# Optimization experiments

Hardware: AMD Instinct MI355X
Metric: run time of the kernel (lower is better)

## Reference

```python
import jax, jax.numpy as jnp
import numpy as np
from jax import lax

L, B, T, C, F = 4, 4, 2048, 1024, 4096  # n_layer, batch, ctx_len, n_embd(=dim_att), dim_ffn
EPS = 1e-5


def setup_inputs() -> dict:
    key = jax.random.key(0)
    ks = jax.random.split(key, 16)
    s = 0.02
    d = {}
    d["x"] = jax.random.normal(ks[0], (B, T, C), jnp.float32)
    d["ln0_w"] = jnp.ones((C,), jnp.float32)
    d["ln0_b"] = jnp.zeros((C,), jnp.float32)
    d["ln1_w"] = jnp.ones((L, C), jnp.float32)
    d["ln1_b"] = jnp.zeros((L, C), jnp.float32)
    d["ln2_w"] = jnp.ones((L, C), jnp.float32)
    d["ln2_b"] = jnp.zeros((L, C), jnp.float32)
    d["time_decay"] = jax.random.normal(ks[1], (L, C), jnp.float32) * 0.5
    d["time_first"] = jax.random.normal(ks[2], (L, C), jnp.float32) * 0.5 + jnp.float32(np.log(0.3))
    d["tmk"] = jax.random.uniform(ks[3], (L, C), jnp.float32)
    d["tmv"] = jax.random.uniform(ks[4], (L, C), jnp.float32)
    d["tmr"] = jax.random.uniform(ks[5], (L, C), jnp.float32)
    d["Wk"] = jax.random.normal(ks[6], (L, C, C), jnp.float32) * s
    d["Wv"] = jax.random.normal(ks[7], (L, C, C), jnp.float32) * s
    d["Wr"] = jax.random.normal(ks[8], (L, C, C), jnp.float32) * s
    d["Wo"] = jax.random.normal(ks[9], (L, C, C), jnp.float32) * s
    d["cmk"] = jax.random.uniform(ks[10], (L, C), jnp.float32)
    d["cmr"] = jax.random.uniform(ks[11], (L, C), jnp.float32)
    d["Wck"] = jax.random.normal(ks[12], (L, F, C), jnp.float32) * s  # key: n_embd -> dim_ffn
    d["Wcv"] = jax.random.normal(ks[13], (L, C, F), jnp.float32) * s  # value: dim_ffn -> n_embd
    d["Wcr"] = jax.random.normal(ks[14], (L, C, C), jnp.float32) * s  # receptance
    return d


def layernorm(x, w, b):
    m = jnp.mean(x, axis=-1, keepdims=True)
    v = jnp.var(x, axis=-1, keepdims=True)
    return (x - m) * lax.rsqrt(v + EPS) * w + b


def time_shift(x):
    # ZeroPad2d((0,0,1,-1)): shift sequence right by one, zero at t=0
    return jnp.pad(x, ((0, 0), (1, 0), (0, 0)))[:, :-1]


def wkv(time_decay, time_first, k, v):
    # numerically-stable RWKV-4 WKV recurrence; k,v: [B,T,C]
    w = -jnp.exp(time_decay)  # [C]
    u = time_first            # [C]
    kt = jnp.swapaxes(k, 0, 1)  # [T,B,C]
    vt = jnp.swapaxes(v, 0, 1)
    Bn, Cn = k.shape[0], k.shape[2]
    init = (jnp.zeros((Bn, Cn), k.dtype), jnp.zeros((Bn, Cn), k.dtype),
            jnp.full((Bn, Cn), -1e38, k.dtype))

    def step(carry, kv):
        aa, bb, pp = carry
        kk, vv = kv
        ww = u + kk
        qq = jnp.maximum(pp, ww)
        e1 = jnp.exp(pp - qq)
        e2 = jnp.exp(ww - qq)
        out = (e1 * aa + e2 * vv) / (e1 * bb + e2)
        ww2 = pp + w
        qq2 = jnp.maximum(ww2, kk)
        e1b = jnp.exp(ww2 - qq2)
        e2b = jnp.exp(kk - qq2)
        return (e1b * aa + e2b * vv, e1b * bb + e2b, qq2), out

    _, out = lax.scan(step, init, (kt, vt))
    return jnp.swapaxes(out, 0, 1)  # [B,T,C]


def reference(x, ln0_w, ln0_b, ln1_w, ln1_b, ln2_w, ln2_b, time_decay, time_first,
              tmk, tmv, tmr, Wk, Wv, Wr, Wo, cmk, cmr, Wck, Wcv, Wcr):
    x = layernorm(x, ln0_w, ln0_b)  # ln0 on layer 0
    for l in range(L):
        # --- TimeMix ---
        h = layernorm(x, ln1_w[l], ln1_b[l])
        hh = time_shift(h)
        xk = h * tmk[l] + hh * (1 - tmk[l])
        xv = h * tmv[l] + hh * (1 - tmv[l])
        xr = h * tmr[l] + hh * (1 - tmr[l])
        k = jnp.einsum('btc,oc->bto', xk, Wk[l])
        v = jnp.einsum('btc,oc->bto', xv, Wv[l])
        sr = jax.nn.sigmoid(jnp.einsum('btc,oc->bto', xr, Wr[l]))
        rwkv = sr * wkv(time_decay[l], time_first[l], k, v)
        x = x + jnp.einsum('bto,co->btc', rwkv, Wo[l])
        # --- ChannelMix ---
        h = layernorm(x, ln2_w[l], ln2_b[l])
        hh = time_shift(h)
        xk = h * cmk[l] + hh * (1 - cmk[l])
        xr = h * cmr[l] + hh * (1 - cmr[l])
        kf = jnp.einsum('btc,fc->btf', xk, Wck[l])
        kf = jnp.square(jax.nn.relu(kf))
        kv = jnp.einsum('btf,cf->btc', kf, Wcv[l])
        x = x + jax.nn.sigmoid(jnp.einsum('btc,oc->bto', xr, Wcr[l])) * kv
    return x
```

## Files before the change

### kernel.cpp

```cpp
#include <hip/hip_runtime.h>
#include <cstdint>

#define TT 2048
#define CCH 1024
#define FFD 4096
#define EPSV 1e-5f
#define NCHK 32
#define CHKL 64

typedef __attribute__((ext_vector_type(4))) float floatx4;
typedef __attribute__((ext_vector_type(8))) short shortx8;

__device__ __forceinline__ unsigned short f32_to_bf16(float f){
  union { float f; unsigned int u; } x; x.f = f;
  unsigned int r = x.u + 0x7fffu + ((x.u >> 16) & 1u);
  return (unsigned short)(r >> 16);
}
__device__ __forceinline__ float bf16_to_f32(unsigned short h){
  union { unsigned int u; float f; } x; x.u = ((unsigned int)h) << 16;
  return x.f;
}
__device__ __forceinline__ float wave_sum(float v){
  #pragma unroll
  for (int o = 32; o > 0; o >>= 1) v += __shfl_down(v, o, 64);
  return v;
}
__device__ __forceinline__ void async16(const void* g, void* l){
  __builtin_amdgcn_global_load_lds((const __attribute__((address_space(1))) void*)g,
                                   (__attribute__((address_space(3))) void*)l, 16, 0, 0);
}

__global__ __launch_bounds__(256) void cvt_kernel(const float* __restrict__ s,
                                                  unsigned short* __restrict__ d, int n4){
  int i = blockIdx.x * 256 + threadIdx.x;
  if (i >= n4) return;
  float4 v = ((const float4*)s)[i];
  union { unsigned short u[4]; uint2 p; } o;
  o.u[0] = f32_to_bf16(v.x); o.u[1] = f32_to_bf16(v.y);
  o.u[2] = f32_to_bf16(v.z); o.u[3] = f32_to_bf16(v.w);
  *(uint2*)&d[(long)i * 4] = o.p;
}

__global__ __launch_bounds__(256) void ln0_kernel(const float* __restrict__ xin,
    const float* __restrict__ w, const float* __restrict__ b, float* __restrict__ xo){
  const int row = blockIdx.x, tid = threadIdx.x;
  const float* xr = xin + (long)row * CCH;
  float c4[4]; float s = 0.f, s2 = 0.f;
  #pragma unroll
  for (int j = 0; j < 4; j++){ c4[j] = xr[tid + j*256]; s += c4[j]; s2 += c4[j]*c4[j]; }
  s = wave_sum(s); s2 = wave_sum(s2);
  __shared__ float red[2][4];
  const int wid = tid >> 6, lane = tid & 63;
  if (lane == 0){ red[0][wid] = s; red[1][wid] = s2; }
  __syncthreads();
  const float S  = red[0][0]+red[0][1]+red[0][2]+red[0][3];
  const float S2 = red[1][0]+red[1][1]+red[1][2]+red[1][3];
  const float inv = 1.f / CCH;
  const float m = S * inv;
  const float rs = rsqrtf(S2 * inv - m*m + EPSV);
  float* xout = xo + (long)row * CCH;
  #pragma unroll
  for (int j = 0; j < 4; j++){ int c = tid + j*256; xout[c] = (c4[j]-m)*rs*w[c] + b[c]; }
}

template<int NOUT>
__global__ __launch_bounds__(256) void ln_mix(
    const float* __restrict__ x,
    const float* __restrict__ lw, const float* __restrict__ lb,
    const float* __restrict__ mk, const float* __restrict__ mv, const float* __restrict__ mr,
    unsigned short* __restrict__ xk, unsigned short* __restrict__ xv, unsigned short* __restrict__ xr)
{
  const int row = blockIdx.x;
  const int t = row & (TT - 1);
  const int tid = threadIdx.x;
  const float* xc = x + (long)row * CCH;
  const float* xp = xc - CCH;
  float c4[4], p4[4];
  float s1=0.f, s2=0.f, s3=0.f, s4=0.f;
  #pragma unroll
  for (int j = 0; j < 4; j++){
    const int c = tid + j*256;
    c4[j] = xc[c];
    p4[j] = (t > 0) ? xp[c] : 0.f;
    s1 += c4[j]; s2 += c4[j]*c4[j];
    s3 += p4[j]; s4 += p4[j]*p4[j];
  }
  s1 = wave_sum(s1); s2 = wave_sum(s2); s3 = wave_sum(s3); s4 = wave_sum(s4);
  __shared__ float red[4][4];
  const int wid = tid >> 6, lane = tid & 63;
  if (lane == 0){ red[wid][0]=s1; red[wid][1]=s2; red[wid][2]=s3; red[wid][3]=s4; }
  __syncthreads();
  const float S1 = red[0][0]+red[1][0]+red[2][0]+red[3][0];
  const float S2 = red[0][1]+red[1][1]+red[2][1]+red[3][1];
  const float S3 = red[0][2]+red[1][2]+red[2][2]+red[3][2];
  const float S4 = red[0][3]+red[1][3]+red[2][3]+red[3][3];
  const float inv = 1.f / CCH;
  const float m1 = S1*inv; const float r1 = rsqrtf(S2*inv - m1*m1 + EPSV);
  const float m0 = S3*inv; const float r0 = rsqrtf(S4*inv - m0*m0 + EPSV);
  #pragma unroll
  for (int j = 0; j < 4; j++){
    const int c = tid + j*256;
    const long o = (long)row * CCH + c;
    const float wv = lw[c], bv = lb[c];
    const float h  = (c4[j]-m1)*r1*wv + bv;
    const float hp = (t > 0) ? ((p4[j]-m0)*r0*wv + bv) : 0.f;
    const float a = mk[c]; xk[o] = f32_to_bf16(h*a + hp*(1.f-a));
    if (NOUT == 3){ const float q = mv[c]; xv[o] = f32_to_bf16(h*q + hp*(1.f-q)); }
    const float g = mr[c]; xr[o] = f32_to_bf16(h*g + hp*(1.f-g));
  }
}

__global__ __launch_bounds__(256) void wkv_pass1(
    const unsigned short* __restrict__ kin, const unsigned short* __restrict__ vin,
    const float* __restrict__ td,
    float* __restrict__ sta, float* __restrict__ stb, float* __restrict__ stp)
{
  const int c = blockIdx.x * 256 + threadIdx.x;
  const int chunk = blockIdx.y, b = blockIdx.z;
  const float w = -__expf(td[c]);
  const long base = ((long)b * TT + (long)chunk * CHKL) * CCH + c;
  float aa = 0.f, bb = 0.f, pp = -1e38f;
  for (int t0 = 0; t0 < CHKL; t0 += 8) {
    float kr[8], vr[8];
    #pragma unroll
    for (int j = 0; j < 8; j++){
      const long o = base + (long)(t0 + j) * CCH;
      kr[j] = bf16_to_f32(kin[o]);
      vr[j] = bf16_to_f32(vin[o]);
    }
    #pragma unroll
    for (int j = 0; j < 8; j++){
      const float kk = kr[j], vv = vr[j];
      const float ww2 = pp + w;
      const float qq2 = fmaxf(ww2, kk);
      const float e1b = __expf(ww2 - qq2), e2b = __expf(kk - qq2);
      aa = e1b*aa + e2b*vv; bb = e1b*bb + e2b; pp = qq2;
    }
  }
  const long si = (long)chunk * 4096 + b * CCH + c;
  sta[si] = aa; stb[si] = bb; stp[si] = pp;
}

__global__ __launch_bounds__(256) void wkv_combine(
    const float* __restrict__ td,
    const float* __restrict__ sta, const float* __restrict__ stb, const float* __restrict__ stp,
    float* __restrict__ ina, float* __restrict__ inb, float* __restrict__ inp)
{
  const int idx = blockIdx.x * 256 + threadIdx.x;
  const int c = idx & (CCH - 1);
  const float wn = -__expf(td[c]) * (float)CHKL;
  float a = 0.f, b = 0.f, p = -1e38f;
  for (int j0 = 0; j0 < NCHK; j0 += 8) {
    float la[8], lb[8], lp[8];
    #pragma unroll
    for (int j = 0; j < 8; j++){
      const long si = (long)(j0 + j) * 4096 + idx;
      la[j] = sta[si]; lb[j] = stb[si]; lp[j] = stp[si];
    }
    #pragma unroll
    for (int j = 0; j < 8; j++){
      const long si = (long)(j0 + j) * 4096 + idx;
      ina[si] = a; inb[si] = b; inp[si] = p;
      const float pd = p + wn;
      const float q = fmaxf(pd, lp[j]);
      const float e1 = __expf(pd - q), e2 = __expf(lp[j] - q);
      a = e1*a + e2*la[j]; b = e1*b + e2*lb[j]; p = q;
    }
  }
}

__global__ __launch_bounds__(256) void wkv_pass2(
    const unsigned short* __restrict__ kin, const unsigned short* __restrict__ vin,
    const unsigned short* __restrict__ srin,
    const float* __restrict__ td, const float* __restrict__ tf,
    const float* __restrict__ ina, const float* __restrict__ inb, const float* __restrict__ inp,
    unsigned short* __restrict__ out)
{
  const int c = blockIdx.x * 256 + threadIdx.x;
  const int chunk = blockIdx.y, b = blockIdx.z;
  const float w = -__expf(td[c]);
  const float u = tf[c];
  const long si = (long)chunk * 4096 + b * CCH + c;
  float aa = ina[si], bb = inb[si], pp = inp[si];
  const long base = ((long)b * TT + (long)chunk * CHKL) * CCH + c;
  for (int t0 = 0; t0 < CHKL; t0 += 8) {
    float kr[8], vr[8], sr[8];
    #pragma unroll
    for (int j = 0; j < 8; j++){
      const long o = base + (long)(t0 + j) * CCH;
      kr[j] = bf16_to_f32(kin[o]);
      vr[j] = bf16_to_f32(vin[o]);
      sr[j] = bf16_to_f32(srin[o]);
    }
    #pragma unroll
    for (int j = 0; j < 8; j++){
      const float kk = kr[j], vv = vr[j];
      const float ww = u + kk;
      const float qq = fmaxf(pp, ww);
      const float e1 = __expf(pp - qq), e2 = __expf(ww - qq);
      const float outv = (e1*aa + e2*vv) / (e1*bb + e2);
      const float ww2 = pp + w;
      const float qq2 = fmaxf(ww2, kk);
      const float e1b = __expf(ww2 - qq2), e2b = __expf(kk - qq2);
      aa = e1b*aa + e2b*vv; bb = e1b*bb + e2b; pp = qq2;
      out[base + (long)(t0 + j) * CCH] = f32_to_bf16(sr[j] * outv);
    }
  }
}

#define BM 128
#define BN 128
#define BK 32

enum { EP_BF16 = 0, EP_SIG = 1, EP_RELU2 = 2, EP_ADD = 3, EP_MULADD = 4 };

template<int EPI>
__global__ __launch_bounds__(256) void gemm_bt(
    const unsigned short* __restrict__ A,
    const unsigned short* __restrict__ W,
    const int N, const int K,
    unsigned short* __restrict__ outb,
    float* __restrict__ xres,
    const unsigned short* __restrict__ rr)
{
  __shared__ unsigned short lA[BM * BK];
  __shared__ unsigned short lW[BN * BK];
  const int tid = threadIdx.x;
  const int bm = blockIdx.x, bn = blockIdx.y;
  const int wid = tid >> 6, lane = tid & 63;
  const int wm = (wid >> 1) * 64, wn = (wid & 1) * 64;
  const int quad = lane >> 4, r16 = lane & 15;

  const unsigned short* Ag = A + ((long)(bm * BM + (tid >> 2))) * K + (tid & 3) * 8;
  const unsigned short* Wg = W + ((long)(bn * BN + (tid >> 2))) * K + (tid & 3) * 8;
  const long rs64 = (long)64 * K;
  unsigned short* lA0 = &lA[wid * 512];
  unsigned short* lA1 = &lA[2048 + wid * 512];
  unsigned short* lW0 = &lW[wid * 512];
  unsigned short* lW1 = &lW[2048 + wid * 512];

  const floatx4 zf = {0.f, 0.f, 0.f, 0.f};
  floatx4 acc[4][4];
  #pragma unroll
  for (int i = 0; i < 4; i++)
    #pragma unroll
    for (int j = 0; j < 4; j++) acc[i][j] = zf;

  for (int k0 = 0; k0 < K; k0 += BK) {
    __syncthreads();
    async16(Ag + k0, lA0);
    async16(Ag + rs64 + k0, lA1);
    async16(Wg + k0, lW0);
    async16(Wg + rs64 + k0, lW1);
    __syncthreads();
    shortx8 af[4], bf[4];
    #pragma unroll
    for (int m = 0; m < 4; m++) af[m] = *(const shortx8*)&lA[(wm + m*16 + r16) * BK + quad * 8];
    #pragma unroll
    for (int n = 0; n < 4; n++) bf[n] = *(const shortx8*)&lW[(wn + n*16 + r16) * BK + quad * 8];
    #pragma unroll
    for (int m = 0; m < 4; m++)
      #pragma unroll
      for (int n = 0; n < 4; n++)
        acc[m][n] = __builtin_amdgcn_mfma_f32_16x16x32_bf16(af[m], bf[n], acc[m][n], 0, 0, 0);
  }

  const int colBase = bn * BN + wn + r16;
  #pragma unroll
  for (int m = 0; m < 4; m++) {
    const int rowBase = bm * BM + wm + m * 16 + quad * 4;
    #pragma unroll
    for (int n = 0; n < 4; n++) {
      const int col = colBase + n * 16;
      #pragma unroll
      for (int r = 0; r < 4; r++) {
        const long idx = (long)(rowBase + r) * N + col;
        const float val = acc[m][n][r];
        if (EPI == EP_BF16)      outb[idx] = f32_to_bf16(val);
        else if (EPI == EP_SIG)  outb[idx] = f32_to_bf16(1.f / (1.f + __expf(-val)));
        else if (EPI == EP_RELU2){ const float t = val > 0.f ? val : 0.f; outb[idx] = f32_to_bf16(t * t); }
        else if (EPI == EP_ADD)  xres[idx] += val;
        else                     xres[idx] = fmaf(bf16_to_f32(rr[idx]), val, xres[idx]);
      }
    }
  }
}

extern "C" void kernel_launch(void* const* d_in, const int* in_sizes, int n_in,
                              void* d_out, int out_size, void* d_ws, size_t ws_size,
                              hipStream_t stream)
{
  const float* x_in       = (const float*)d_in[0];
  const float* ln0_w      = (const float*)d_in[1];
  const float* ln0_b      = (const float*)d_in[2];
  const float* ln1_w      = (const float*)d_in[3];
  const float* ln1_b      = (const float*)d_in[4];
  const float* ln2_w      = (const float*)d_in[5];
  const float* ln2_b      = (const float*)d_in[6];
  const float* time_decay = (const float*)d_in[7];
  const float* time_first = (const float*)d_in[8];
  const float* tmk        = (const float*)d_in[9];
  const float* tmv        = (const float*)d_in[10];
  const float* tmr        = (const float*)d_in[11];
  const float* Wk         = (const float*)d_in[12];
  const float* Wv         = (const float*)d_in[13];
  const float* Wr         = (const float*)d_in[14];
  const float* Wo         = (const float*)d_in[15];
  const float* cmk        = (const float*)d_in[16];
  const float* cmr        = (const float*)d_in[17];
  const float* Wck        = (const float*)d_in[18];
  const float* Wcv        = (const float*)d_in[19];
  const float* Wcr        = (const float*)d_in[20];
  float* x = (float*)d_out;

  const int M = 4 * TT;
  const long lCC = (long)CCH * CCH;
  const long lFC = (long)FFD * CCH;
  const long MC  = (long)M * CCH;

  unsigned short* wsl  = (unsigned short*)d_ws;
  unsigned short* wkb  = wsl;
  unsigned short* wvb  = wkb + lCC;
  unsigned short* wrb  = wvb + lCC;
  unsigned short* wob  = wrb + lCC;
  unsigned short* wcrb = wob + lCC;
  unsigned short* wckb = wcrb + lCC;
  unsigned short* wcvb = wckb + lFC;
  unsigned short* xk   = wcvb + lFC;
  unsigned short* xv   = xk + MC;
  unsigned short* xr   = xv + MC;
  unsigned short* kbuf = xr + MC;
  unsigned short* vbuf = kbuf + MC;
  unsigned short* sbuf = vbuf + MC;
  unsigned short* kfb  = kbuf;
  unsigned short* rrb  = kbuf + (long)M * FFD;

  float* stf = (float*)xk;
  float* sta = stf;
  float* stb = sta + (long)NCHK * 4096;
  float* stp = stb + (long)NCHK * 4096;
  float* ina = stp + (long)NCHK * 4096;
  float* inb = ina + (long)NCHK * 4096;
  float* inp = inb + (long)NCHK * 4096;

  auto cvt = [&](const float* s, unsigned short* d, long n){
    int n4 = (int)(n / 4);
    cvt_kernel<<<(n4 + 255) / 256, 256, 0, stream>>>(s, d, n4);
  };

  ln0_kernel<<<M, 256, 0, stream>>>(x_in, ln0_w, ln0_b, x);

  const dim3 g1(M / BM, CCH / BN);
  const dim3 g2(M / BM, FFD / BN);
  const dim3 gw(CCH / 256, NCHK, 4);

  for (int l = 0; l < 4; l++) {
    cvt(Wk  + (long)l * lCC, wkb,  lCC);
    cvt(Wv  + (long)l * lCC, wvb,  lCC);
    cvt(Wr  + (long)l * lCC, wrb,  lCC);
    cvt(Wo  + (long)l * lCC, wob,  lCC);
    cvt(Wcr + (long)l * lCC, wcrb, lCC);
    cvt(Wck + (long)l * lFC, wckb, lFC);
    cvt(Wcv + (long)l * lFC, wcvb, lFC);

    const float* td_l = time_decay + l*CCH;
    const float* tf_l = time_first + l*CCH;

    ln_mix<3><<<M, 256, 0, stream>>>(x, ln1_w + l*CCH, ln1_b + l*CCH,
                                     tmk + l*CCH, tmv + l*CCH, tmr + l*CCH, xk, xv, xr);
    gemm_bt<EP_BF16><<<g1, 256, 0, stream>>>(xk, wkb, CCH, CCH, kbuf, nullptr, nullptr);
    gemm_bt<EP_BF16><<<g1, 256, 0, stream>>>(xv, wvb, CCH, CCH, vbuf, nullptr, nullptr);
    gemm_bt<EP_SIG ><<<g1, 256, 0, stream>>>(xr, wrb, CCH, CCH, sbuf, nullptr, nullptr);
    wkv_pass1 <<<gw, 256, 0, stream>>>(kbuf, vbuf, td_l, sta, stb, stp);
    wkv_combine<<<16, 256, 0, stream>>>(td_l, sta, stb, stp, ina, inb, inp);
    wkv_pass2 <<<gw, 256, 0, stream>>>(kbuf, vbuf, sbuf, td_l, tf_l, ina, inb, inp, xv);
    gemm_bt<EP_ADD ><<<g1, 256, 0, stream>>>(xv, wob, CCH, CCH, nullptr, x, nullptr);

    ln_mix<2><<<M, 256, 0, stream>>>(x, ln2_w + l*CCH, ln2_b + l*CCH,
                                     cmk + l*CCH, nullptr, cmr + l*CCH, xk, nullptr, xr);
    gemm_bt<EP_SIG   ><<<g1, 256, 0, stream>>>(xr, wcrb, CCH, CCH, rrb, nullptr, nullptr);
    gemm_bt<EP_RELU2 ><<<g2, 256, 0, stream>>>(xk, wckb, FFD, CCH, kfb, nullptr, nullptr);
    gemm_bt<EP_MULADD><<<g1, 256, 0, stream>>>(kfb, wcvb, CCH, FFD, nullptr, x, rrb);
  }
}
```

Measured before the change: 2.004 ms.

## Batch weight conversions, widen GEMM K-tile with swizzled LDS, fuse K/V/R GEMMs

Replaces the seven per-weight conversion launches with a single multi-segment conversion kernel. Doubles the GEMM K-tile to 64 and stores the LDS tiles with an XOR swizzle, which halves the number of K-loop barriers and aims to avoid LDS bank conflicts. Merges the three TimeMix K/V/R projections into one z-batched launch that relies on contiguous xk/xv/xr, weight and output buffers, with the sigmoid applied only for the receptance slice. The larger tile doubles LDS use per block, which may reduce occupancy.

```diff
diff --git a/kernel.cpp b/kernel.cpp
--- a/kernel.cpp
+++ b/kernel.cpp
@@ -30,15 +30,23 @@
                                    (__attribute__((address_space(3))) void*)l, 16, 0, 0);
 }
 
-__global__ __launch_bounds__(256) void cvt_kernel(const float* __restrict__ s,
-                                                  unsigned short* __restrict__ d, int n4){
-  int i = blockIdx.x * 256 + threadIdx.x;
-  if (i >= n4) return;
-  float4 v = ((const float4*)s)[i];
-  union { unsigned short u[4]; uint2 p; } o;
-  o.u[0] = f32_to_bf16(v.x); o.u[1] = f32_to_bf16(v.y);
-  o.u[2] = f32_to_bf16(v.z); o.u[3] = f32_to_bf16(v.w);
-  *(uint2*)&d[(long)i * 4] = o.p;
+struct CvtArgs {
+  const float* s[7];
+  unsigned short* d[7];
+  int n4[7];
+};
+__global__ __launch_bounds__(256) void cvt7_kernel(CvtArgs a){
+  const int seg = blockIdx.y;
+  const float* __restrict__ s = a.s[seg];
+  unsigned short* __restrict__ d = a.d[seg];
+  const int n4 = a.n4[seg];
+  for (int i = blockIdx.x * 256 + threadIdx.x; i < n4; i += gridDim.x * 256) {
+    float4 v = ((const float4*)s)[i];
+    union { unsigned short u[4]; uint2 p; } o;
+    o.u[0] = f32_to_bf16(v.x); o.u[1] = f32_to_bf16(v.y);
+    o.u[2] = f32_to_bf16(v.z); o.u[3] = f32_to_bf16(v.w);
+    *(uint2*)&d[(long)i * 4] = o.p;
+  }
 }
 
 __global__ __launch_bounds__(256) void ln0_kernel(const float* __restrict__ xin,
@@ -210,9 +218,9 @@
 
 #define BM 128
 #define BN 128
-#define BK 32
-
-enum { EP_BF16 = 0, EP_SIG = 1, EP_RELU2 = 2, EP_ADD = 3, EP_MULADD = 4 };
+#define BK 64
+
+enum { EP_BF16 = 0, EP_SIG = 1, EP_RELU2 = 2, EP_ADD = 3, EP_MULADD = 4, EP_KVR = 5 };
 
 template<int EPI>
 __global__ __launch_bounds__(256) void gemm_bt(
@@ -223,6 +231,13 @@
     float* __restrict__ xres,
     const unsigned short* __restrict__ rr)
 {
+  if (EPI == EP_KVR) {
+    const long z = blockIdx.z;
+    const long Mfull = (long)gridDim.x * BM;
+    A    += z * Mfull * K;
+    W    += z * (long)N * K;
+    outb += z * Mfull * N;
+  }
   __shared__ unsigned short lA[BM * BK];
   __shared__ unsigned short lW[BN * BK];
   const int tid = threadIdx.x;
@@ -231,13 +246,14 @@
   const int wm = (wid >> 1) * 64, wn = (wid & 1) * 64;
   const int quad = lane >> 4, r16 = lane & 15;
 
-  const unsigned short* Ag = A + ((long)(bm * BM + (tid >> 2))) * K + (tid & 3) * 8;
-  const unsigned short* Wg = W + ((long)(bn * BN + (tid >> 2))) * K + (tid & 3) * 8;
-  const long rs64 = (long)64 * K;
-  unsigned short* lA0 = &lA[wid * 512];
-  unsigned short* lA1 = &lA[2048 + wid * 512];
-  unsigned short* lW0 = &lW[wid * 512];
-  unsigned short* lW1 = &lW[2048 + wid * 512];
+  const int srow = tid >> 3;
+  const int scol = (tid & 7) ^ (srow & 7);
+  const unsigned short* Ag = A + ((long)(bm * BM + srow)) * K + scol * 8;
+  const unsigned short* Wg = W + ((long)(bn * BN + srow)) * K + scol * 8;
+  const long rs32 = (long)32 * K;
+
+  const int sw0 = ((quad)     ^ (r16 & 7)) * 8;
+  const int sw1 = ((4 + quad) ^ (r16 & 7)) * 8;
 
   const floatx4 zf = {0.f, 0.f, 0.f, 0.f};
   floatx4 acc[4][4];
@@ -248,21 +264,26 @@
 
   for (int k0 = 0; k0 < K; k0 += BK) {
     __syncthreads();
-    async16(Ag + k0, lA0);
-    async16(Ag + rs64 + k0, lA1);
-    async16(Wg + k0, lW0);
-    async16(Wg + rs64 + k0, lW1);
+    #pragma unroll
+    for (int i = 0; i < 4; i++) {
+      async16(Ag + (long)i * rs32 + k0, &lA[(i * 256 + wid * 64) * 8]);
+      async16(Wg + (long)i * rs32 + k0, &lW[(i * 256 + wid * 64) * 8]);
+    }
     __syncthreads();
-    shortx8 af[4], bf[4];
-    #pragma unroll
-    for (int m = 0; m < 4; m++) af[m] = *(const shortx8*)&lA[(wm + m*16 + r16) * BK + quad * 8];
-    #pragma unroll
-    for (int n = 0; n < 4; n++) bf[n] = *(const shortx8*)&lW[(wn + n*16 + r16) * BK + quad * 8];
-    #pragma unroll
-    for (int m = 0; m < 4; m++)
+    #pragma unroll
+    for (int kk = 0; kk < 2; kk++) {
+      const int sw = kk ? sw1 : sw0;
+      shortx8 af[4], bf[4];
       #pragma unroll
-      for (int n = 0; n < 4; n++)
-        acc[m][n] = __builtin_amdgcn_mfma_f32_16x16x32_bf16(af[m], bf[n], acc[m][n], 0, 0, 0);
+      for (int m = 0; m < 4; m++) af[m] = *(const shortx8*)&lA[(wm + m*16 + r16) * 64 + sw];
+      #pragma unroll
+      for (int n = 0; n < 4; n++) bf[n] = *(const shortx8*)&lW[(wn + n*16 + r16) * 64 + sw];
+      #pragma unroll
+      for (int m = 0; m < 4; m++)
+        #pragma unroll
+        for (int n = 0; n < 4; n++)
+          acc[m][n] = __builtin_amdgcn_mfma_f32_16x16x32_bf16(af[m], bf[n], acc[m][n], 0, 0, 0);
+    }
   }
 
   const int colBase = bn * BN + wn + r16;
@@ -277,6 +298,9 @@
         const long idx = (long)(rowBase + r) * N + col;
         const float val = acc[m][n][r];
         if (EPI == EP_BF16)      outb[idx] = f32_to_bf16(val);
+        else if (EPI == EP_KVR)  outb[idx] = (blockIdx.z == 2)
+                                   ? f32_to_bf16(1.f / (1.f + __expf(-val)))
+                                   : f32_to_bf16(val);
         else if (EPI == EP_SIG)  outb[idx] = f32_to_bf16(1.f / (1.f + __expf(-val)));
         else if (EPI == EP_RELU2){ const float t = val > 0.f ? val : 0.f; outb[idx] = f32_to_bf16(t * t); }
         else if (EPI == EP_ADD)  xres[idx] += val;
@@ -335,42 +359,37 @@
   unsigned short* kfb  = kbuf;
   unsigned short* rrb  = kbuf + (long)M * FFD;
 
-  float* stf = (float*)xk;
-  float* sta = stf;
+  float* sta = (float*)xk;
   float* stb = sta + (long)NCHK * 4096;
   float* stp = stb + (long)NCHK * 4096;
   float* ina = stp + (long)NCHK * 4096;
   float* inb = ina + (long)NCHK * 4096;
   float* inp = inb + (long)NCHK * 4096;
 
-  auto cvt = [&](const float* s, unsigned short* d, long n){
-    int n4 = (int)(n / 4);
-    cvt_kernel<<<(n4 + 255) / 256, 256, 0, stream>>>(s, d, n4);
-  };
-
   ln0_kernel<<<M, 256, 0, stream>>>(x_in, ln0_w, ln0_b, x);
 
   const dim3 g1(M / BM, CCH / BN);
   const dim3 g2(M / BM, FFD / BN);
+  const dim3 gkvr(M / BM, CCH / BN, 3);
   const dim3 gw(CCH / 256, NCHK, 4);
 
   for (int l = 0; l < 4; l++) {
-    cvt(Wk  + (long)l * lCC, wkb,  lCC);
-    cvt(Wv  + (long)l * lCC, wvb,  lCC);
-    cvt(Wr  + (long)l * lCC, wrb,  lCC);
-    cvt(Wo  + (long)l * lCC, wob,  lCC);
-    cvt(Wcr + (long)l * lCC, wcrb, lCC);
-    cvt(Wck + (long)l * lFC, wckb, lFC);
-    cvt(Wcv + (long)l * lFC, wcvb, lFC);
+    CvtArgs ca;
+    ca.s[0] = Wk  + (long)l * lCC; ca.d[0] = wkb;  ca.n4[0] = (int)(lCC / 4);
+    ca.s[1] = Wv  + (long)l * lCC; ca.d[1] = wvb;  ca.n4[1] = (int)(lCC / 4);
+    ca.s[2] = Wr  + (long)l * lCC; ca.d[2] = wrb;  ca.n4[2] = (int)(lCC / 4);
+    ca.s[3] = Wo  + (long)l * lCC; ca.d[3] = wob;  ca.n4[3] = (int)(lCC / 4);
+    ca.s[4] = Wcr + (long)l * lCC; ca.d[4] = wcrb; ca.n4[4] = (int)(lCC / 4);
+    ca.s[5] = Wck + (long)l * lFC; ca.d[5] = wckb; ca.n4[5] = (int)(lFC / 4);
+    ca.s[6] = Wcv + (long)l * lFC; ca.d[6] = wcvb; ca.n4[6] = (int)(lFC / 4);
+    cvt7_kernel<<<dim3(512, 7), 256, 0, stream>>>(ca);
 
     const float* td_l = time_decay + l*CCH;
     const float* tf_l = time_first + l*CCH;
 
     ln_mix<3><<<M, 256, 0, stream>>>(x, ln1_w + l*CCH, ln1_b + l*CCH,
                                      tmk + l*CCH, tmv + l*CCH, tmr + l*CCH, xk, xv, xr);
-    gemm_bt<EP_BF16><<<g1, 256, 0, stream>>>(xk, wkb, CCH, CCH, kbuf, nullptr, nullptr);
-    gemm_bt<EP_BF16><<<g1, 256, 0, stream>>>(xv, wvb, CCH, CCH, vbuf, nullptr, nullptr);
-    gemm_bt<EP_SIG ><<<g1, 256, 0, stream>>>(xr, wrb, CCH, CCH, sbuf, nullptr, nullptr);
+    gemm_bt<EP_KVR><<<gkvr, 256, 0, stream>>>(xk, wkb, CCH, CCH, kbuf, nullptr, nullptr);
     wkv_pass1 <<<gw, 256, 0, stream>>>(kbuf, vbuf, td_l, sta, stb, stp);
     wkv_combine<<<16, 256, 0, stream>>>(td_l, sta, stb, stp, ina, inb, inp);
     wkv_pass2 <<<gw, 256, 0, stream>>>(kbuf, vbuf, sbuf, td_l, tf_l, ina, inb, inp, xv);
```

After: 1.711 ms. 14.6% less time.
